# Performance work log

Measured on AMD Instinct MI355X. Metric: run time of the kernel, lower is better.

The kernel has to match this reference:

```python
import jax, jax.numpy as jnp
import numpy as np

EPS = 1e-5
NUM_GROUPS = 32
NUM_HEADS = 4


def setup_inputs() -> dict:
    key = jax.random.key(0)
    ks = jax.random.split(key, 3)
    B, C, H, W = 4, 256, 64, 64
    x = jax.random.normal(ks[0], (B, C, H, W), dtype=jnp.float32)
    gn_w = jnp.ones((C,), jnp.float32)
    gn_b = jnp.zeros((C,), jnp.float32)
    qkv_w = jax.random.normal(ks[1], (3 * C, C), dtype=jnp.float32) * (C ** -0.5)
    qkv_b = jnp.zeros((3 * C,), jnp.float32)
    proj_w = jax.random.normal(ks[2], (C, C), dtype=jnp.float32) * (C ** -0.5)
    proj_b = jnp.zeros((C,), jnp.float32)
    return {"x": x, "gn_w": gn_w, "gn_b": gn_b, "qkv_w": qkv_w,
            "qkv_b": qkv_b, "proj_w": proj_w, "proj_b": proj_b}


def _group_norm(x, w, b):
    B, C, H, W = x.shape
    xg = x.reshape(B, NUM_GROUPS, C // NUM_GROUPS, H, W)
    mean = xg.mean(axis=(2, 3, 4), keepdims=True)
    var = xg.var(axis=(2, 3, 4), keepdims=True)
    xn = ((xg - mean) * jax.lax.rsqrt(var + EPS)).reshape(B, C, H, W)
    return xn * w[None, :, None, None] + b[None, :, None, None]


def reference(x, gn_w, gn_b, qkv_w, qkv_b, proj_w, proj_b):
    B, C, H, W = x.shape
    nh = NUM_HEADS
    d = C // nh
    L = H * W
    h = _group_norm(x, gn_w, gn_b)
    # 1x1 conv == channel matmul
    qkv = jnp.einsum('oc,bchw->bohw', qkv_w, h) + qkv_b[None, :, None, None]
    q, k, v = jnp.split(qkv, 3, axis=1)
    # (B, C, H, W) -> (B, nh, L, d)
    def to_heads(t):
        return t.reshape(B, nh, d, L).transpose(0, 1, 3, 2)
    q, k, v = to_heads(q), to_heads(k), to_heads(v)
    scale = d ** -0.5
    attn = jax.nn.softmax(jnp.einsum('bhqd,bhkd->bhqk', q, k) * scale, axis=-1)
    o = jnp.einsum('bhqk,bhkd->bhqd', attn, v)          # (B, nh, L, d)
    o = o.transpose(0, 1, 3, 2).reshape(B, C, H, W)
    o = jnp.einsum('oc,bchw->bohw', proj_w, o) + proj_b[None, :, None, None]
    return x + o
```

## Files before the change

kernel.cpp:

```cpp
#include <hip/hip_runtime.h>

#define B_   4
#define C_   256
#define L_   4096
#define NH_  4
#define D_   64
#define G_   32
#define CPG_ 8

typedef __bf16 bf16x8 __attribute__((ext_vector_type(8)));
typedef float  f32x4  __attribute__((ext_vector_type(4)));

__device__ __forceinline__ ushort f2bf(float f) {
  union { float f; unsigned u; } c; c.f = f;
  unsigned u = c.u;
  return (ushort)((u + 0x7fffu + ((u >> 16) & 1u)) >> 16);
}
__device__ __forceinline__ float bf2f(ushort h) {
  union { unsigned u; float f; } c; c.u = ((unsigned)h) << 16; return c.f;
}
__device__ __forceinline__ unsigned fbits(float f) {
  union { float f; unsigned u; } c; c.f = f; return c.u;
}
__device__ __forceinline__ float fastexp2(float x) {
#if __has_builtin(__builtin_amdgcn_exp2f)
  return __builtin_amdgcn_exp2f(x);
#else
  return exp2f(x);
#endif
}

__global__ __launch_bounds__(256) void pre_kernel(const float* __restrict__ x,
                                                  const float* __restrict__ wqf,
                                                  const float* __restrict__ wpf,
                                                  ushort* __restrict__ wq,
                                                  ushort* __restrict__ wp,
                                                  float* __restrict__ stats2) {
  int bidx = blockIdx.x;
  int tid  = threadIdx.x;
  if (bidx >= 1024) {
    int t = (bidx - 1024) * 256 + tid;
    const int NQ4 = (768 * 256) / 4;
    float4 v;
    if (t < NQ4) {
      v = ((const float4*)wqf)[t];
      ((ushort4*)wq)[t] = make_ushort4(f2bf(v.x), f2bf(v.y), f2bf(v.z), f2bf(v.w));
    } else {
      int i = t - NQ4;
      v = ((const float4*)wpf)[i];
      ((ushort4*)wp)[i] = make_ushort4(f2bf(v.x), f2bf(v.y), f2bf(v.z), f2bf(v.w));
    }
    return;
  }
  int bg = bidx >> 3, chunk = bidx & 7;
  int b = bg >> 5, g = bg & 31;
  const float* xg = x + ((size_t)b * C_ + g * CPG_) * L_ + chunk * 512;

  float s = 0.f, ss = 0.f;
  for (int c = 0; c < CPG_; ++c) {
    float2 v = ((const float2*)(xg + (size_t)c * L_))[tid];
    s  += v.x + v.y;
    ss += v.x * v.x + v.y * v.y;
  }
  for (int off = 32; off; off >>= 1) { s += __shfl_xor(s, off); ss += __shfl_xor(ss, off); }
  __shared__ float red[8];
  int w = tid >> 6;
  if ((tid & 63) == 0) { red[w] = s; red[4 + w] = ss; }
  __syncthreads();
  if (tid == 0) {
    stats2[bidx * 2]     = red[0] + red[1] + red[2] + red[3];
    stats2[bidx * 2 + 1] = red[4] + red[5] + red[6] + red[7];
  }
}

__global__ __launch_bounds__(256) void gn_apply(const float* __restrict__ x,
                                                const float* __restrict__ gw,
                                                const float* __restrict__ gb,
                                                const float* __restrict__ stats2,
                                                ushort* __restrict__ hT) {
  int bid = blockIdx.x;
  int b     = bid >> 7;
  int lslab = (bid & 127) >> 3;
  int cslab = bid & 7;
  int tid = threadIdx.x;
  int l0 = lslab * 256, c0 = cslab * 32;

  const float inv_n = 1.0f / (CPG_ * L_);
  float mean[4], rstd[4];
#pragma unroll
  for (int gg = 0; gg < 4; ++gg) {
    int bg = b * 32 + cslab * 4 + gg;
    float s = 0.f, ss = 0.f;
#pragma unroll
    for (int c2 = 0; c2 < 8; ++c2) {
      s  += stats2[(bg * 8 + c2) * 2];
      ss += stats2[(bg * 8 + c2) * 2 + 1];
    }
    mean[gg] = s * inv_n;
    float var = ss * inv_n - mean[gg] * mean[gg];
    rstd[gg] = rsqrtf(var + 1e-5f);
  }

  int l = l0 + tid;
  union { uint4 u[4]; ushort s[32]; } o;
#pragma unroll
  for (int c = 0; c < 32; ++c) {
    int gg = c >> 3;
    float wv = gw[c0 + c], bv = gb[c0 + c];
    float v = x[((size_t)b * C_ + c0 + c) * L_ + l];
    o.s[c] = f2bf((v - mean[gg]) * rstd[gg] * wv + bv);
  }
  ushort* dst = hT + ((size_t)b * L_ + l) * C_ + c0;
#pragma unroll
  for (int i = 0; i < 4; ++i)
    ((uint4*)dst)[i] = o.u[i];
}

__global__ __launch_bounds__(256) void qkv_kernel(const ushort* __restrict__ hT,
                                                  const ushort* __restrict__ w,
                                                  const float* __restrict__ bias,
                                                  ushort* __restrict__ q,
                                                  ushort* __restrict__ k,
                                                  ushort* __restrict__ v) {
  int wid  = blockIdx.x * 4 + (threadIdx.x >> 6);
  int lane = threadIdx.x & 63;
  int quad = lane >> 4, col = lane & 15;
  int ot   = wid % 12;
  int rest = wid / 12;
  int lt   = rest & 127;
  int b    = rest >> 7;
  int o0 = ot * 64, l0 = lt * 32;

  const ushort* abase = w  + (size_t)(o0 + col) * C_ + quad * 8;
  const ushort* bbase = hT + ((size_t)b * L_ + l0 + col) * C_ + quad * 8;

  f32x4 acc[4][2];
  for (int i = 0; i < 4; ++i) for (int j = 0; j < 2; ++j)
    acc[i][j] = (f32x4){0.f, 0.f, 0.f, 0.f};

#pragma unroll
  for (int k0 = 0; k0 < C_; k0 += 32) {
    bf16x8 a[4], bb[2];
#pragma unroll
    for (int i = 0; i < 4; ++i) a[i]  = *(const bf16x8*)(abase + (size_t)(i * 16) * C_ + k0);
#pragma unroll
    for (int j = 0; j < 2; ++j) bb[j] = *(const bf16x8*)(bbase + (size_t)(j * 16) * C_ + k0);
#pragma unroll
    for (int i = 0; i < 4; ++i)
#pragma unroll
      for (int j = 0; j < 2; ++j)
        acc[i][j] = __builtin_amdgcn_mfma_f32_16x16x32_bf16(a[i], bb[j], acc[i][j], 0, 0, 0);
  }

  int third = o0 >> 8;
  int hh    = (o0 & 255) >> 6;
  float scale = (third == 0) ? 0.180336880111120f : 1.0f;
#pragma unroll
  for (int i = 0; i < 4; ++i) {
    int oo = o0 + i * 16 + quad * 4;
    int dd = i * 16 + quad * 4;
#pragma unroll
    for (int j = 0; j < 2; ++j) {
      int l = l0 + j * 16 + col;
      ushort pk[4];
      for (int r = 0; r < 4; ++r) pk[r] = f2bf((acc[i][j][r] + bias[oo + r]) * scale);
      if (third < 2) {
        ushort* dst = (third ? k : q) + (((size_t)(b * NH_ + hh) * L_ + l) * D_ + dd);
        *(ushort4*)dst = make_ushort4(pk[0], pk[1], pk[2], pk[3]);
      } else {
        for (int r = 0; r < 4; ++r)
          v[((size_t)(b * NH_ + hh) * D_ + dd + r) * L_ + l] = pk[r];
      }
    }
  }
}

__global__ __launch_bounds__(256, 2) void attn_kernel(const ushort* __restrict__ q,
                                                      const ushort* __restrict__ k,
                                                      const ushort* __restrict__ v,
                                                      ushort* __restrict__ p0,
                                                      ushort* __restrict__ p1,
                                                      float* __restrict__ psumbuf) {
  __shared__ __align__(16) ushort k_lds[2][64][72];
  __shared__ __align__(16) ushort v_lds[2][64][72];

  int tid   = threadIdx.x;
  int w     = tid >> 6, lane = tid & 63;
  int quad  = lane >> 4, col = lane & 15;
  int bid   = (int)blockIdx.x;
  bid = (bid & 7) * 64 + (bid >> 3);
  int split = bid >> 8;
  int bh    = (bid >> 4) & 15;
  int qblk  = bid & 15;

  const ushort* qp = q + (size_t)bh * L_ * D_;
  const ushort* kp = k + (size_t)bh * L_ * D_;
  const ushort* vp = v + (size_t)bh * D_ * L_;

  int qrow0 = qblk * 256 + w * 64;
  bf16x8 bq[4][2];
#pragma unroll
  for (int f = 0; f < 4; ++f)
#pragma unroll
    for (int c = 0; c < 2; ++c)
      bq[f][c] = *(const bf16x8*)(qp + (size_t)(qrow0 + f * 16 + col) * D_ + c * 32 + quad * 8);

  f32x4 oacc[4][4];
#pragma unroll
  for (int f = 0; f < 4; ++f)
    for (int t = 0; t < 4; ++t) oacc[f][t] = (f32x4){0.f, 0.f, 0.f, 0.f};
  f32x4 pacc[4];
#pragma unroll
  for (int f = 0; f < 4; ++f) pacc[f] = (f32x4){0.f, 0.f, 0.f, 0.f};
  const f32x4 Z = (f32x4){0.f, 0.f, 0.f, 0.f};

  union { ushort s[8]; bf16x8 v8; } one_u;
#pragma unroll
  for (int i = 0; i < 8; ++i) one_u.s[i] = 0x3F80;
  bf16x8 ones = one_u.v8;

  int vrow = tid >> 2, vchunk = tid & 3;
  int vwoff = (vchunk >> 1) * 32 + (vchunk & 1) * 4;
  int kt0 = split * (L_ / 2), kt_end = kt0 + L_ / 2;

  {
    const uint4* ksrc = (const uint4*)(kp + (size_t)kt0 * D_);
    uint4 a  = ksrc[tid];
    uint4 b2 = ksrc[tid + 256];
    const uint4* vsrc = (const uint4*)(vp + (size_t)vrow * L_ + kt0);
    uint4 c0 = vsrc[vchunk * 2];
    uint4 c1 = vsrc[vchunk * 2 + 1];
    *(uint4*)&k_lds[0][tid >> 3][(tid & 7) * 8] = a;
    *(uint4*)&k_lds[0][32 + (tid >> 3)][(tid & 7) * 8] = b2;
    ushort* vb = &v_lds[0][vrow][vwoff];
    *(uint2*)(vb + 0)  = make_uint2(c0.x, c0.y);
    *(uint2*)(vb + 8)  = make_uint2(c0.z, c0.w);
    *(uint2*)(vb + 16) = make_uint2(c1.x, c1.y);
    *(uint2*)(vb + 24) = make_uint2(c1.z, c1.w);
  }
  __syncthreads();

  int cur = 0;
  for (int kt = kt0; kt < kt_end; kt += 64) {
    bool has_next = (kt + 64) < kt_end;

    f32x4 s[2][4][2];
#pragma unroll
    for (int h = 0; h < 2; ++h) {
      bf16x8 a00 = *(const bf16x8*)&k_lds[cur][h * 32 + col][quad * 8];
      bf16x8 a01 = *(const bf16x8*)&k_lds[cur][h * 32 + col][32 + quad * 8];
      bf16x8 a10 = *(const bf16x8*)&k_lds[cur][h * 32 + 16 + col][quad * 8];
      bf16x8 a11 = *(const bf16x8*)&k_lds[cur][h * 32 + 16 + col][32 + quad * 8];
#pragma unroll
      for (int f = 0; f < 4; ++f) {
        s[h][f][0] = __builtin_amdgcn_mfma_f32_16x16x32_bf16(a00, bq[f][0], Z, 0, 0, 0);
        s[h][f][1] = __builtin_amdgcn_mfma_f32_16x16x32_bf16(a10, bq[f][0], Z, 0, 0, 0);
        s[h][f][0] = __builtin_amdgcn_mfma_f32_16x16x32_bf16(a01, bq[f][1], s[h][f][0], 0, 0, 0);
        s[h][f][1] = __builtin_amdgcn_mfma_f32_16x16x32_bf16(a11, bq[f][1], s[h][f][1], 0, 0, 0);
      }
    }

    uint4 nk0, nk1, nv0, nv1;
    if (has_next) {
      const uint4* ksrc = (const uint4*)(kp + (size_t)(kt + 64) * D_);
      nk0 = ksrc[tid];
      nk1 = ksrc[tid + 256];
      const uint4* vsrc = (const uint4*)(vp + (size_t)vrow * L_ + (kt + 64));
      nv0 = vsrc[vchunk * 2];
      nv1 = vsrc[vchunk * 2 + 1];
    }

#pragma unroll
    for (int h = 0; h < 2; ++h) {
      bf16x8 pb[4];
#pragma unroll
      for (int f = 0; f < 4; ++f) {
        float pe0[4], pe1[4];
#pragma unroll
        for (int r = 0; r < 4; ++r) {
          pe0[r] = fastexp2(s[h][f][0][r]);
          pe1[r] = fastexp2(s[h][f][1][r]);
        }
        union { unsigned u[4]; bf16x8 v8; } pc;
        pc.u[0] = __builtin_amdgcn_perm(fbits(pe0[1]), fbits(pe0[0]), 0x07060302u);
        pc.u[1] = __builtin_amdgcn_perm(fbits(pe0[3]), fbits(pe0[2]), 0x07060302u);
        pc.u[2] = __builtin_amdgcn_perm(fbits(pe1[1]), fbits(pe1[0]), 0x07060302u);
        pc.u[3] = __builtin_amdgcn_perm(fbits(pe1[3]), fbits(pe1[2]), 0x07060302u);
        pb[f] = pc.v8;
      }
#pragma unroll
      for (int f = 0; f < 4; ++f)
        pacc[f] = __builtin_amdgcn_mfma_f32_16x16x32_bf16(ones, pb[f], pacc[f], 0, 0, 0);
#pragma unroll
      for (int t = 0; t < 4; ++t) {
        bf16x8 av = *(const bf16x8*)&v_lds[cur][t * 16 + col][h * 32 + quad * 8];
#pragma unroll
        for (int f = 0; f < 4; ++f)
          oacc[f][t] = __builtin_amdgcn_mfma_f32_16x16x32_bf16(av, pb[f], oacc[f][t], 0, 0, 0);
      }
    }

    if (has_next) {
      int nb = cur ^ 1;
      *(uint4*)&k_lds[nb][tid >> 3][(tid & 7) * 8] = nk0;
      *(uint4*)&k_lds[nb][32 + (tid >> 3)][(tid & 7) * 8] = nk1;
      ushort* vb = &v_lds[nb][vrow][vwoff];
      *(uint2*)(vb + 0)  = make_uint2(nv0.x, nv0.y);
      *(uint2*)(vb + 8)  = make_uint2(nv0.z, nv0.w);
      *(uint2*)(vb + 16) = make_uint2(nv1.x, nv1.y);
      *(uint2*)(vb + 24) = make_uint2(nv1.z, nv1.w);
      __syncthreads();
      cur = nb;
    }
  }

  ushort* po = split ? p1 : p0;
#pragma unroll
  for (int f = 0; f < 4; ++f) {
    for (int t = 0; t < 4; ++t) {
      ushort ok[4];
      for (int r = 0; r < 4; ++r) ok[r] = f2bf(oacc[f][t][r]);
      ushort* dst = po + ((size_t)bh * L_ + qrow0 + f * 16 + col) * D_ + t * 16 + quad * 4;
      *(ushort4*)dst = make_ushort4(ok[0], ok[1], ok[2], ok[3]);
    }
    if (quad == 0)
      psumbuf[split * (16 * L_) + bh * L_ + qrow0 + f * 16 + col] = pacc[f][0];
  }
}

__global__ __launch_bounds__(256) void comb_kernel(ushort* __restrict__ p0,
                                                   const ushort* __restrict__ p1,
                                                   const float* __restrict__ ps) {
  int idx = blockIdx.x * 256 + threadIdx.x;
  int row = idx >> 3;
  float inv = 1.0f / (ps[row] + ps[16 * L_ + row]);
  union { uint4 u; ushort s[8]; } ua, ub, o;
  ua.u = ((const uint4*)p0)[idx];
  ub.u = ((const uint4*)p1)[idx];
#pragma unroll
  for (int e = 0; e < 8; ++e)
    o.s[e] = f2bf((bf2f(ua.s[e]) + bf2f(ub.s[e])) * inv);
  ((uint4*)p0)[idx] = o.u;
}

template<bool FUSED>
__global__ __launch_bounds__(256) void proj_kernel(const ushort* __restrict__ p0,
                                                   const ushort* __restrict__ p1,
                                                   const float* __restrict__ ps,
                                                   const ushort* __restrict__ pw,
                                                   const float* __restrict__ pb,
                                                   const float* __restrict__ x,
                                                   float* __restrict__ out) {
  __shared__ __align__(16) ushort a_lds[32][264];

  int tid  = threadIdx.x;
  int w    = tid >> 6, lane = tid & 63;
  int quad = lane >> 4, col = lane & 15;
  int bid  = (int)blockIdx.x;
  int oct  = (bid & 1) * 4 + w;
  int lt   = (bid >> 1) & 127;
  int b    = bid >> 8;
  int l0 = lt * 32, oc0 = oct * 32;

  if (FUSED) {
    int ll = tid & 31, chunk = tid >> 5;
    int hh = chunk >> 1, d0 = (chunk & 1) * 32;
    size_t row = (size_t)(b * NH_ + hh) * L_ + l0 + ll;
    float inv = 1.0f / (ps[row] + ps[16 * L_ + row]);
    const uint4* s0 = (const uint4*)(p0 + row * D_ + d0);
    const uint4* s1 = (const uint4*)(p1 + row * D_ + d0);
    union { uint4 u[4]; ushort s[32]; } ua, ub, o;
#pragma unroll
    for (int i = 0; i < 4; ++i) { ua.u[i] = s0[i]; ub.u[i] = s1[i]; }
#pragma unroll
    for (int e = 0; e < 32; ++e)
      o.s[e] = f2bf((bf2f(ua.s[e]) + bf2f(ub.s[e])) * inv);
#pragma unroll
    for (int i = 0; i < 4; ++i)
      *(uint4*)&a_lds[ll][chunk * 32 + i * 8] = o.u[i];
    __syncthreads();
  }

  f32x4 acc[2][2];
  for (int i = 0; i < 2; ++i) for (int j = 0; j < 2; ++j)
    acc[i][j] = (f32x4){0.f, 0.f, 0.f, 0.f};

#pragma unroll
  for (int k0 = 0; k0 < C_; k0 += 32) {
    int hh = k0 >> 6, dk = k0 & 63;
    bf16x8 a[2], bb[2];
#pragma unroll
    for (int i = 0; i < 2; ++i) {
      if (FUSED) {
        a[i] = *(const bf16x8*)&a_lds[i * 16 + col][k0 + quad * 8];
      } else {
        a[i] = *(const bf16x8*)(p0 + ((size_t)(b * NH_ + hh) * L_ + l0 + i * 16 + col) * D_ + dk + quad * 8);
      }
    }
#pragma unroll
    for (int j = 0; j < 2; ++j)
      bb[j] = *(const bf16x8*)(pw + (size_t)(oc0 + j * 16 + col) * C_ + k0 + quad * 8);
#pragma unroll
    for (int i = 0; i < 2; ++i)
#pragma unroll
      for (int j = 0; j < 2; ++j)
        acc[i][j] = __builtin_amdgcn_mfma_f32_16x16x32_bf16(a[i], bb[j], acc[i][j], 0, 0, 0);
  }

#pragma unroll
  for (int j = 0; j < 2; ++j) {
    int oc = oc0 + j * 16 + col;
    float bias = pb[oc];
#pragma unroll
    for (int i = 0; i < 2; ++i) {
      int l = l0 + i * 16 + quad * 4;
      size_t off = ((size_t)b * C_ + oc) * L_ + l;
      float4 xv = *(const float4*)(x + off);
      float4 ov = make_float4(acc[i][j][0] + bias + xv.x,
                              acc[i][j][1] + bias + xv.y,
                              acc[i][j][2] + bias + xv.z,
                              acc[i][j][3] + bias + xv.w);
      *(float4*)(out + off) = ov;
    }
  }
}

extern "C" void kernel_launch(void* const* d_in, const int* in_sizes, int n_in,
                              void* d_out, int out_size, void* d_ws, size_t ws_size,
                              hipStream_t stream) {
  const float* x      = (const float*)d_in[0];
  const float* gn_w   = (const float*)d_in[1];
  const float* gn_b   = (const float*)d_in[2];
  const float* qkv_w  = (const float*)d_in[3];
  const float* qkv_b  = (const float*)d_in[4];
  const float* proj_w = (const float*)d_in[5];
  const float* proj_b = (const float*)d_in[6];
  float* out = (float*)d_out;

  const size_t TEN = (size_t)B_ * C_ * L_;
  ushort* ws  = (ushort*)d_ws;
  ushort* q   = ws;
  ushort* k   = ws + TEN;
  ushort* v   = ws + 2 * TEN;
  ushort* oat = ws + 3 * TEN;
  ushort* wq  = ws + 4 * TEN;
  ushort* wp  = wq + 768 * 256;
  ushort* wend = wp + 256 * 256;
  ushort* hT  = (ushort*)d_out;
  float*  st2 = (float*)((ushort*)d_out + TEN);

  const size_t base_bytes  = (size_t)(wend - ws) * 2;
  const size_t need_fused  = base_bytes + TEN * 2  + (size_t)2 * 16 * L_ * 4 ;
  const bool   fused       = ws_size >= need_fused;

  pre_kernel <<<1280,      256, 0, stream>>>(x, qkv_w, proj_w, wq, wp, st2);
  gn_apply   <<<512,       256, 0, stream>>>(x, gn_w, gn_b, st2, hT);
  qkv_kernel <<<6144 / 4,  256, 0, stream>>>(hT, wq, qkv_b, q, k, v);

  if (fused) {
    ushort* p1w = wend;
    float*  psw = (float*)(wend + TEN);
    attn_kernel<<<512, 256, 0, stream>>>(q, k, v, oat, p1w, psw);
    proj_kernel<true><<<1024, 256, 0, stream>>>(oat, p1w, psw, wp, proj_b, x, out);
  } else {
    ushort* p1d = (ushort*)d_out + TEN;
    float*  psb = (float*)d_out;
    attn_kernel<<<512, 256, 0, stream>>>(q, k, v, oat, p1d, psb);
    comb_kernel<<<2048, 256, 0, stream>>>(oat, p1d, psb);
    proj_kernel<false><<<1024, 256, 0, stream>>>(oat, oat, psb, wp, proj_b, x, out);
  }
}
```

Baseline: 206.4 us.

## Fuse GroupNorm apply into QKV projection via LDS-staged normalized tile

Removes the separate gn_apply kernel and its hT round trip through global memory. Each QKV block now normalizes a 32-position slab of x for all 256 channels into shared memory, and each wave then computes three output tiles reading B operands from LDS. Separately, the attention kernel raises wave priority around the QK^T MFMA section. The grid shrinks from 1536 to 512 blocks, each doing more serial work, which may reduce occupancy and latency hiding.

```diff
diff --git a/kernel.cpp b/kernel.cpp
--- a/kernel.cpp
+++ b/kernel.cpp
@@ -73,103 +73,101 @@
   }
 }
 
-__global__ __launch_bounds__(256) void gn_apply(const float* __restrict__ x,
-                                                const float* __restrict__ gw,
-                                                const float* __restrict__ gb,
-                                                const float* __restrict__ stats2,
-                                                ushort* __restrict__ hT) {
-  int bid = blockIdx.x;
-  int b     = bid >> 7;
-  int lslab = (bid & 127) >> 3;
-  int cslab = bid & 7;
-  int tid = threadIdx.x;
-  int l0 = lslab * 256, c0 = cslab * 32;
-
-  const float inv_n = 1.0f / (CPG_ * L_);
-  float mean[4], rstd[4];
-#pragma unroll
-  for (int gg = 0; gg < 4; ++gg) {
-    int bg = b * 32 + cslab * 4 + gg;
-    float s = 0.f, ss = 0.f;
-#pragma unroll
-    for (int c2 = 0; c2 < 8; ++c2) {
-      s  += stats2[(bg * 8 + c2) * 2];
-      ss += stats2[(bg * 8 + c2) * 2 + 1];
-    }
-    mean[gg] = s * inv_n;
-    float var = ss * inv_n - mean[gg] * mean[gg];
-    rstd[gg] = rsqrtf(var + 1e-5f);
-  }
-
-  int l = l0 + tid;
-  union { uint4 u[4]; ushort s[32]; } o;
-#pragma unroll
-  for (int c = 0; c < 32; ++c) {
-    int gg = c >> 3;
-    float wv = gw[c0 + c], bv = gb[c0 + c];
-    float v = x[((size_t)b * C_ + c0 + c) * L_ + l];
-    o.s[c] = f2bf((v - mean[gg]) * rstd[gg] * wv + bv);
-  }
-  ushort* dst = hT + ((size_t)b * L_ + l) * C_ + c0;
-#pragma unroll
-  for (int i = 0; i < 4; ++i)
-    ((uint4*)dst)[i] = o.u[i];
-}
-
-__global__ __launch_bounds__(256) void qkv_kernel(const ushort* __restrict__ hT,
+__global__ __launch_bounds__(256) void qkv_kernel(const float* __restrict__ x,
+                                                  const float* __restrict__ stats2,
+                                                  const float* __restrict__ gw,
+                                                  const float* __restrict__ gb,
                                                   const ushort* __restrict__ w,
                                                   const float* __restrict__ bias,
                                                   ushort* __restrict__ q,
                                                   ushort* __restrict__ k,
                                                   ushort* __restrict__ v) {
-  int wid  = blockIdx.x * 4 + (threadIdx.x >> 6);
-  int lane = threadIdx.x & 63;
+  __shared__ __align__(16) ushort h_lds[32][264];
+
+  int tid  = threadIdx.x;
+  int wv_  = tid >> 6, lane = tid & 63;
   int quad = lane >> 4, col = lane & 15;
-  int ot   = wid % 12;
-  int rest = wid / 12;
-  int lt   = rest & 127;
-  int b    = rest >> 7;
-  int o0 = ot * 64, l0 = lt * 32;
-
-  const ushort* abase = w  + (size_t)(o0 + col) * C_ + quad * 8;
-  const ushort* bbase = hT + ((size_t)b * L_ + l0 + col) * C_ + quad * 8;
-
-  f32x4 acc[4][2];
-  for (int i = 0; i < 4; ++i) for (int j = 0; j < 2; ++j)
-    acc[i][j] = (f32x4){0.f, 0.f, 0.f, 0.f};
-
-#pragma unroll
-  for (int k0 = 0; k0 < C_; k0 += 32) {
-    bf16x8 a[4], bb[2];
-#pragma unroll
-    for (int i = 0; i < 4; ++i) a[i]  = *(const bf16x8*)(abase + (size_t)(i * 16) * C_ + k0);
-#pragma unroll
-    for (int j = 0; j < 2; ++j) bb[j] = *(const bf16x8*)(bbase + (size_t)(j * 16) * C_ + k0);
+  int bid  = (int)blockIdx.x;
+  int b    = bid >> 7;
+  int lt   = bid & 127;
+  int l0   = lt * 32;
+
+  {
+    int ll = tid & 31, chunk = tid >> 5;
+    int c0 = chunk * 32;
+    const float inv_n = 1.0f / (CPG_ * L_);
+    float mean[4], rstd[4];
+#pragma unroll
+    for (int gg = 0; gg < 4; ++gg) {
+      int bg = b * 32 + chunk * 4 + gg;
+      float s = 0.f, ss = 0.f;
+#pragma unroll
+      for (int c2 = 0; c2 < 8; ++c2) {
+        s  += stats2[(bg * 8 + c2) * 2];
+        ss += stats2[(bg * 8 + c2) * 2 + 1];
+      }
+      mean[gg] = s * inv_n;
+      float var = ss * inv_n - mean[gg] * mean[gg];
+      rstd[gg] = rsqrtf(var + 1e-5f);
+    }
+    int l = l0 + ll;
+    union { uint4 u[4]; ushort s[32]; } o;
+#pragma unroll
+    for (int c = 0; c < 32; ++c) {
+      int gg = c >> 3;
+      float wvv = gw[c0 + c], bvv = gb[c0 + c];
+      float val = x[((size_t)b * C_ + c0 + c) * L_ + l];
+      o.s[c] = f2bf((val - mean[gg]) * rstd[gg] * wvv + bvv);
+    }
 #pragma unroll
     for (int i = 0; i < 4; ++i)
-#pragma unroll
-      for (int j = 0; j < 2; ++j)
-        acc[i][j] = __builtin_amdgcn_mfma_f32_16x16x32_bf16(a[i], bb[j], acc[i][j], 0, 0, 0);
-  }
-
-  int third = o0 >> 8;
-  int hh    = (o0 & 255) >> 6;
-  float scale = (third == 0) ? 0.180336880111120f : 1.0f;
-#pragma unroll
-  for (int i = 0; i < 4; ++i) {
-    int oo = o0 + i * 16 + quad * 4;
-    int dd = i * 16 + quad * 4;
-#pragma unroll
-    for (int j = 0; j < 2; ++j) {
-      int l = l0 + j * 16 + col;
-      ushort pk[4];
-      for (int r = 0; r < 4; ++r) pk[r] = f2bf((acc[i][j][r] + bias[oo + r]) * scale);
-      if (third < 2) {
-        ushort* dst = (third ? k : q) + (((size_t)(b * NH_ + hh) * L_ + l) * D_ + dd);
-        *(ushort4*)dst = make_ushort4(pk[0], pk[1], pk[2], pk[3]);
-      } else {
-        for (int r = 0; r < 4; ++r)
-          v[((size_t)(b * NH_ + hh) * D_ + dd + r) * L_ + l] = pk[r];
+      *(uint4*)&h_lds[ll][c0 + i * 8] = o.u[i];
+  }
+  __syncthreads();
+
+#pragma unroll
+  for (int p = 0; p < 3; ++p) {
+    int ot = wv_ + 4 * p;
+    int o0 = ot * 64;
+    const ushort* abase = w + (size_t)(o0 + col) * C_ + quad * 8;
+
+    f32x4 acc[4][2];
+    for (int i = 0; i < 4; ++i) for (int j = 0; j < 2; ++j)
+      acc[i][j] = (f32x4){0.f, 0.f, 0.f, 0.f};
+
+#pragma unroll
+    for (int k0 = 0; k0 < C_; k0 += 32) {
+      bf16x8 a[4], bb[2];
+#pragma unroll
+      for (int i = 0; i < 4; ++i) a[i]  = *(const bf16x8*)(abase + (size_t)(i * 16) * C_ + k0);
+#pragma unroll
+      for (int j = 0; j < 2; ++j) bb[j] = *(const bf16x8*)&h_lds[j * 16 + col][k0 + quad * 8];
+#pragma unroll
+      for (int i = 0; i < 4; ++i)
+#pragma unroll
+        for (int j = 0; j < 2; ++j)
+          acc[i][j] = __builtin_amdgcn_mfma_f32_16x16x32_bf16(a[i], bb[j], acc[i][j], 0, 0, 0);
+    }
+
+    int third = o0 >> 8;
+    int hh    = (o0 & 255) >> 6;
+    float scale = (third == 0) ? 0.180336880111120f : 1.0f;
+#pragma unroll
+    for (int i = 0; i < 4; ++i) {
+      int oo = o0 + i * 16 + quad * 4;
+      int dd = i * 16 + quad * 4;
+#pragma unroll
+      for (int j = 0; j < 2; ++j) {
+        int l = l0 + j * 16 + col;
+        ushort pk[4];
+        for (int r = 0; r < 4; ++r) pk[r] = f2bf((acc[i][j][r] + bias[oo + r]) * scale);
+        if (third < 2) {
+          ushort* dst = (third ? k : q) + (((size_t)(b * NH_ + hh) * L_ + l) * D_ + dd);
+          *(ushort4*)dst = make_ushort4(pk[0], pk[1], pk[2], pk[3]);
+        } else {
+          for (int r = 0; r < 4; ++r)
+            v[((size_t)(b * NH_ + hh) * D_ + dd + r) * L_ + l] = pk[r];
+        }
       }
     }
   }
@@ -245,6 +243,7 @@
     bool has_next = (kt + 64) < kt_end;
 
     f32x4 s[2][4][2];
+    __builtin_amdgcn_s_setprio(1);
 #pragma unroll
     for (int h = 0; h < 2; ++h) {
       bf16x8 a00 = *(const bf16x8*)&k_lds[cur][h * 32 + col][quad * 8];
@@ -259,6 +258,7 @@
         s[h][f][1] = __builtin_amdgcn_mfma_f32_16x16x32_bf16(a11, bq[f][1], s[h][f][1], 0, 0, 0);
       }
     }
+    __builtin_amdgcn_s_setprio(0);
 
     uint4 nk0, nk1, nv0, nv1;
     if (has_next) {
@@ -446,7 +446,6 @@
   ushort* wq  = ws + 4 * TEN;
   ushort* wp  = wq + 768 * 256;
   ushort* wend = wp + 256 * 256;
-  ushort* hT  = (ushort*)d_out;
   float*  st2 = (float*)((ushort*)d_out + TEN);
 
   const size_t base_bytes  = (size_t)(wend - ws) * 2;
@@ -454,8 +453,7 @@
   const bool   fused       = ws_size >= need_fused;
 
   pre_kernel <<<1280,      256, 0, stream>>>(x, qkv_w, proj_w, wq, wp, st2);
-  gn_apply   <<<512,       256, 0, stream>>>(x, gn_w, gn_b, st2, hT);
-  qkv_kernel <<<6144 / 4,  256, 0, stream>>>(hT, wq, qkv_b, q, k, v);
+  qkv_kernel <<<512,       256, 0, stream>>>(x, st2, gn_w, gn_b, wq, qkv_b, q, k, v);
 
   if (fused) {
     ushort* p1w = wend;
```

Result: faster. 191.5 us (-7.2%).
